# Kernel tuning notes

Hardware: AMD Instinct MI355X
Metric: run time of the kernel (lower is better)

The kernel has to match this reference:

```python
import jax, jax.numpy as jnp
import numpy as np

D_MODEL, D_STATE, EXPAND = 768, 16, 2
D_INNER = D_MODEL * EXPAND
B, L = 2, 2048


def setup_inputs() -> dict:
    key = jax.random.key(0)
    ks = jax.random.split(key, 10)
    s = 0.02  # init scale for projection weights
    return {
        "x": jax.random.normal(ks[0], (B, L, D_MODEL), jnp.float32),
        "in_w": jax.random.normal(ks[1], (D_MODEL, 2 * D_INNER), jnp.float32) * s,
        "conv_w": jax.random.normal(ks[2], (D_INNER, 1, 3), jnp.float32) * 0.1,
        "conv_b": jnp.zeros((D_INNER,), jnp.float32),
        "xproj_w": jax.random.normal(ks[3], (D_INNER, 2 * D_STATE), jnp.float32) * s,
        "dt_w": jax.random.normal(ks[4], (D_INNER, D_INNER), jnp.float32) * s,
        "dt_b": jnp.zeros((D_INNER,), jnp.float32),
        "A_log": jax.random.normal(ks[5], (D_INNER, D_STATE), jnp.float32) * 0.01,
        "D": jnp.ones((D_INNER,), jnp.float32),
        "out_w": jax.random.normal(ks[6], (D_INNER, D_MODEL), jnp.float32) * s,
    }


def reference(x, in_w, conv_w, conv_b, xproj_w, dt_w, dt_b, A_log, D, out_w):
    d_inner = conv_w.shape[0]
    d_state = A_log.shape[1]

    xz = x @ in_w                                   # [B,L,2*d_inner]
    x_c, z = jnp.split(xz, 2, axis=-1)

    # depthwise conv1d, kernel 3, padding 1
    xc = jnp.transpose(x_c, (0, 2, 1))              # [B,d_inner,L]
    xc = jax.lax.conv_general_dilated(
        xc, conv_w, window_strides=(1,), padding=[(1, 1)],
        feature_group_count=d_inner,
        dimension_numbers=("NCH", "OIH", "NCH"))
    xc = xc + conv_b[None, :, None]
    xc = jax.nn.silu(jnp.transpose(xc, (0, 2, 1)))  # [B,L,d_inner]

    Bs, Cs = jnp.split(xc @ xproj_w, 2, axis=-1)    # each [B,L,d_state]
    delta = jax.nn.softplus(xc @ dt_w + dt_b)       # [B,L,d_inner]
    A = -jnp.exp(A_log.astype(jnp.float32))         # [d_inner,d_state]

    deltaA = jnp.exp(jnp.einsum("bld,dn->bldn", delta, A))      # [B,L,d_inner,d_state]
    deltaBx = jnp.einsum("bld,bln->bldn", delta * xc, Bs)        # [B,L,d_inner,d_state]

    def step(h, inp):
        dA_t, dBx_t, c_t = inp                      # [B,d,n],[B,d,n],[B,n]
        h = dA_t * h + dBx_t
        y_t = jnp.einsum("bdn,bn->bd", h, c_t)
        return h, y_t

    h0 = jnp.zeros((x.shape[0], d_inner, d_state), xc.dtype)
    xs = (jnp.moveaxis(deltaA, 1, 0), jnp.moveaxis(deltaBx, 1, 0), jnp.moveaxis(Cs, 1, 0))
    _, ys = jax.lax.scan(step, h0, xs)              # ys: [L,B,d_inner]
    y = jnp.moveaxis(ys, 0, 1) + D * xc             # skip connection

    y = y * jax.nn.silu(z)
    return y @ out_w                                # [B,L,d_model]
```

## Files before the change

kernel.cpp:

```cpp
#include <hip/hip_runtime.h>
#include <cmath>

#define DMODEL 768
#define DINNER 1536
#define NSTATE 16
#define SEQL   2048
#define NCHUNK 32
#define CHLEN  64

#define DT_F32  0
#define DT_BF16 1
#define DT_ZERO 2

typedef __bf16 bf16x8 __attribute__((ext_vector_type(8)));
typedef float  f32x4  __attribute__((ext_vector_type(4)));

typedef __attribute__((address_space(3))) unsigned short lds_us;
typedef const __attribute__((address_space(1))) unsigned short glob_us;

__device__ __forceinline__ void async_cp16(glob_us* g, lds_us* l) {
    __builtin_amdgcn_global_load_lds((const __attribute__((address_space(1))) void*)g,
                                     (__attribute__((address_space(3))) void*)l, 16, 0, 0);
}

__device__ __forceinline__ float bf2f(unsigned short h) {
    union { unsigned u; float f; } v; v.u = ((unsigned)h) << 16; return v.f;
}
__device__ __forceinline__ float bflo(unsigned p) {
    union { unsigned u; float f; } v; v.u = p << 16; return v.f;
}
__device__ __forceinline__ float bfhi(unsigned p) {
    union { unsigned u; float f; } v; v.u = p & 0xFFFF0000u; return v.f;
}
__device__ __forceinline__ unsigned short f2bf(float f) {
    union { float f; unsigned u; } v; v.f = f;
    unsigned r = (v.u + 0x7FFFu + ((v.u >> 16) & 1u)) >> 16;
    return (unsigned short)r;
}
__device__ __forceinline__ float quad_reduce(float y) {
    int yi = __float_as_int(y);
    y += __int_as_float(__builtin_amdgcn_mov_dpp(yi, 0xB1, 0xF, 0xF, true));
    yi = __float_as_int(y);
    y += __int_as_float(__builtin_amdgcn_mov_dpp(yi, 0x4E, 0xF, 0xF, true));
    return y;
}
__device__ int detect_dtype(const void* p) {
    const unsigned* u = (const unsigned*)p;
    int nzlo = 0, band = 0, anynz = 0;
    for (int i = 0; i < 64; ++i) {
        unsigned w = u[i];
        anynz |= (w != 0);
        unsigned lo = w & 0xFFFFu;
        if (lo) {
            ++nzlo;
            unsigned e8 = (lo >> 7) & 0xFF;
            if (e8 >= 0x60 && e8 <= 0x8E) ++band;
        }
    }
    if (nzlo >= 8) return (band * 2 > nzlo) ? DT_BF16 : DT_F32;
    return anynz ? DT_F32 : DT_ZERO;
}
__device__ __forceinline__ float LD(const void* p, size_t i, int dt) {
    if (dt == DT_BF16) return bf2f(((const unsigned short*)p)[i]);
    if (dt == DT_F32)  return ((const float*)p)[i];
    return 0.f;
}

__global__ __launch_bounds__(256) void prep_kernel(
    const void* __restrict__ x, const void* __restrict__ in_w,
    const void* __restrict__ cw, const void* __restrict__ cb,
    const void* __restrict__ xp, const void* __restrict__ dt_w,
    const void* __restrict__ db, const void* __restrict__ Al,
    const void* __restrict__ Dv, const void* __restrict__ out_w,
    unsigned short* __restrict__ xb, unsigned short* __restrict__ inT,
    unsigned short* __restrict__ dtT, unsigned short* __restrict__ outT,
    unsigned short* __restrict__ xpT, float* __restrict__ pf)
{
    __shared__ unsigned short tile[64][68];
    __shared__ int dts[6];
    const int blk = blockIdx.x;
    const int t   = threadIdx.x;

    if (blk < 324) {
        if (t == 0) {
            dts[0] = detect_dtype(cw); dts[1] = detect_dtype(cb);
            dts[2] = detect_dtype(db); dts[3] = detect_dtype(Al);
            dts[4] = detect_dtype(Dv); dts[5] = detect_dtype(xp);
        }
        __syncthreads();
        int g = blk * 256 + t;
        if (g >= 82944) return;
        const void* src; int local; int which;
        if      (g <  4608) { src = cw; local = g;         which = 0; }
        else if (g <  6144) { src = cb; local = g - 4608;  which = 1; }
        else if (g <  7680) { src = db; local = g - 6144;  which = 2; }
        else if (g < 32256) { src = Al; local = g - 7680;  which = 3; }
        else if (g < 33792) { src = Dv; local = g - 32256; which = 4; }
        else                { src = xp; local = g - 33792; which = 5; }
        float v = LD(src, local, dts[which]);
        int out = g;
        if (which == 3) v = -__expf(v) * 1.44269504f;
        if (which == 0) out = (local % 3) * DINNER + local / 3;
        pf[out] = v;
    } else if (blk < 1860) {
        if (t == 0) dts[0] = detect_dtype(x);
        __syncthreads();
        const int dt = dts[0];
        size_t i = ((size_t)(blk - 324) * 256 + t) * 8;
        ushort4 o0, o1;
        if (dt == DT_F32) {
            float4 a = *(const float4*)((const float*)x + i);
            float4 b = *(const float4*)((const float*)x + i + 4);
            o0.x = f2bf(a.x); o0.y = f2bf(a.y); o0.z = f2bf(a.z); o0.w = f2bf(a.w);
            o1.x = f2bf(b.x); o1.y = f2bf(b.y); o1.z = f2bf(b.z); o1.w = f2bf(b.w);
        } else if (dt == DT_BF16) {
            o0 = *(const ushort4*)((const unsigned short*)x + i);
            o1 = *(const ushort4*)((const unsigned short*)x + i + 4);
        } else {
            o0 = (ushort4){0,0,0,0}; o1 = (ushort4){0,0,0,0};
        }
        *(ushort4*)&xb[i] = o0;
        *(ushort4*)&xb[i + 4] = o1;
    } else if (blk < 3300) {
        const void* src; unsigned short* dst; int R, C, tx_n, idx;
        if (blk < 2436)      { src = in_w;  dst = inT;  R = 768;  C = 3072; tx_n = 48; idx = blk - 1860; }
        else if (blk < 3012) { src = dt_w;  dst = dtT;  R = 1536; C = 1536; tx_n = 24; idx = blk - 2436; }
        else                 { src = out_w; dst = outT; R = 1536; C = 768;  tx_n = 12; idx = blk - 3012; }
        if (t == 0) dts[0] = detect_dtype(src);
        __syncthreads();
        const int dt = dts[0];
        const int tx = t & 15, ty = t >> 4;
        const int bx = (idx % tx_n) * 64, by = (idx / tx_n) * 64;
        #pragma unroll
        for (int i = 0; i < 4; ++i) {
            int rl = ty + i * 16;
            size_t soff = (size_t)(by + rl) * C + bx + tx * 4;
            ushort4 hv;
            if (dt == DT_F32) {
                float4 v = *(const float4*)((const float*)src + soff);
                hv.x = f2bf(v.x); hv.y = f2bf(v.y); hv.z = f2bf(v.z); hv.w = f2bf(v.w);
            } else if (dt == DT_BF16) {
                hv = *(const ushort4*)((const unsigned short*)src + soff);
            } else {
                hv = (ushort4){0,0,0,0};
            }
            *(ushort4*)&tile[rl][tx * 4] = hv;
        }
        __syncthreads();
        #pragma unroll
        for (int i = 0; i < 4; ++i) {
            int cl = ty + i * 16;
            int m0 = tx * 4;
            ushort4 o;
            o.x = tile[m0 + 0][cl]; o.y = tile[m0 + 1][cl];
            o.z = tile[m0 + 2][cl]; o.w = tile[m0 + 3][cl];
            *(ushort4*)&dst[(size_t)(bx + cl) * R + by + m0] = o;
        }
    } else {
        if (t == 0) dts[0] = detect_dtype(xp);
        __syncthreads();
        const int dt = dts[0];
        int r = (blk - 3300) * 256 + t;
        #pragma unroll 4
        for (int c = 0; c < 32; ++c) {
            float v = LD(xp, (size_t)r * 32 + c, dt);
            xpT[(size_t)c * DINNER + r] = f2bf(v);
        }
    }
}

template<int EPI>
__global__ __launch_bounds__(256) void gemm_kernel(
    const unsigned short* __restrict__ A, const unsigned short* __restrict__ Bt,
    void* __restrict__ C0, void* __restrict__ C1, const float* __restrict__ biasf,
    int M, int N, int K)
{
    __shared__ __align__(16) unsigned short As[2][2][128 * 32];
    __shared__ __align__(16) unsigned short Bs[2][2][64 * 32];
    const int t    = threadIdx.x;
    const int m0   = blockIdx.x * 128;
    const int n0   = blockIdx.y * 64;
    const int w    = t >> 6;
    const int lane = t & 63;
    const int wm   = (w >> 1) * 64, wn = (w & 1) * 32;
    const int lm   = lane & 15, quad = lane >> 4;
    const int srow = lane >> 2;
    const int sg   = lane & 3;

    f32x4 acc[4][2] = {};

    auto stage = [&](int k0, int q) {
        #pragma unroll
        for (int ph = 0; ph < 2; ++ph) {
            #pragma unroll
            for (int h = 0; h < 2; ++h) {
                int row = w * 32 + h * 16 + srow;
                int kg  = (sg - (row >> 1)) & 3;
                async_cp16((glob_us*)&A[(size_t)(m0 + row) * K + k0 + ph * 32 + kg * 8],
                           (lds_us*)&As[q][ph][(w * 32 + h * 16) * 32]);
            }
            int brow = w * 16 + srow;
            int bkg  = (sg - (brow >> 1)) & 3;
            async_cp16((glob_us*)&Bt[(size_t)(n0 + brow) * K + k0 + ph * 32 + bkg * 8],
                       (lds_us*)&Bs[q][ph][(w * 16) * 32]);
        }
    };

    stage(0, 0);

    int p = 0;
    for (int k0 = 0; k0 < K; k0 += 64) {
        __syncthreads();
        if (k0 + 64 < K) stage(k0 + 64, p ^ 1);
        #pragma unroll
        for (int ph = 0; ph < 2; ++ph) {
            bf16x8 af[4], bfr[2];
            #pragma unroll
            for (int i = 0; i < 4; ++i) {
                int row = wm + i * 16 + lm;
                int g   = (quad + (row >> 1)) & 3;
                af[i] = *(const bf16x8*)&As[p][ph][row * 32 + g * 8];
            }
            #pragma unroll
            for (int j = 0; j < 2; ++j) {
                int row = wn + j * 16 + lm;
                int g   = (quad + (row >> 1)) & 3;
                bfr[j] = *(const bf16x8*)&Bs[p][ph][row * 32 + g * 8];
            }
            #pragma unroll
            for (int i = 0; i < 4; ++i)
                #pragma unroll
                for (int j = 0; j < 2; ++j)
                    acc[i][j] = __builtin_amdgcn_mfma_f32_16x16x32_bf16(af[i], bfr[j], acc[i][j], 0, 0, 0);
        }
        p ^= 1;
    }

    const int half = N >> 1;
    #pragma unroll
    for (int i = 0; i < 4; ++i) {
        #pragma unroll
        for (int j = 0; j < 2; ++j) {
            int col = n0 + wn + j * 16 + lm;
            #pragma unroll
            for (int r = 0; r < 4; ++r) {
                int row = m0 + wm + i * 16 + quad * 4 + r;
                float v = acc[i][j][r];
                if (EPI == 2) {
                    ((float*)C0)[(size_t)row * N + col] = v;
                } else {
                    if (col < half) {
                        ((unsigned short*)C0)[(size_t)row * half + col] = f2bf(v);
                    } else {
                        float s = v / (1.f + __expf(-v));
                        ((unsigned short*)C1)[(size_t)row * half + col - half] = f2bf(s);
                    }
                }
            }
        }
    }
}

__global__ __launch_bounds__(256) void gemm_fused_kernel(
    const unsigned short* __restrict__ A, const unsigned short* __restrict__ Bt,
    const unsigned short* __restrict__ Bt2,
    unsigned short* __restrict__ C0, float* __restrict__ C1,
    const float* __restrict__ biasf, int M, int K)
{
    __shared__ __align__(16) unsigned short As[2][128 * 32];
    __shared__ __align__(16) unsigned short Bs[2][64 * 32];
    const int t    = threadIdx.x;
    const int m0   = blockIdx.x * 128;
    const int n0   = blockIdx.y * 64;
    const int w    = t >> 6;
    const int lane = t & 63;
    const int wm   = (w >> 1) * 64, wn = (w & 1) * 32;
    const int lm   = lane & 15, quad = lane >> 4;
    const int srow = lane >> 2;
    const int sg   = lane & 3;

    const int arow0 = w * 32 + srow;
    const int arow1 = w * 32 + 16 + srow;
    const int akg0  = (sg - (arow0 >> 1)) & 3;
    const int akg1  = (sg - (arow1 >> 1)) & 3;
    const int brow  = w * 16 + srow;
    const int bkg   = (sg - (brow >> 1)) & 3;
    const int gr    = n0 + brow;
    const unsigned short* aB0 = &A[(size_t)(m0 + arow0) * K + akg0 * 8];
    const unsigned short* aB1 = &A[(size_t)(m0 + arow1) * K + akg1 * 8];
    const unsigned short* bB  = (gr < 1536)
        ? &Bt[(size_t)gr * K + bkg * 8]
        : &Bt2[(size_t)(((gr < 1567) ? gr : 1567) - 1536) * K + bkg * 8];

    f32x4 acc[4][2] = {};

    auto stage = [&](int k0, int q) {
        async_cp16((glob_us*)(aB0 + k0), (lds_us*)&As[q][(w * 32) * 32]);
        async_cp16((glob_us*)(aB1 + k0), (lds_us*)&As[q][(w * 32 + 16) * 32]);
        async_cp16((glob_us*)(bB  + k0), (lds_us*)&Bs[q][(w * 16) * 32]);
    };

    stage(0, 0);

    int p = 0;
    for (int k0 = 0; k0 < K; k0 += 32) {
        __syncthreads();
        if (k0 + 32 < K) stage(k0 + 32, p ^ 1);
        bf16x8 af[4], bfr[2];
        #pragma unroll
        for (int i = 0; i < 4; ++i) {
            int row = wm + i * 16 + lm;
            int g   = (quad + (row >> 1)) & 3;
            af[i] = *(const bf16x8*)&As[p][row * 32 + g * 8];
        }
        #pragma unroll
        for (int j = 0; j < 2; ++j) {
            int row = wn + j * 16 + lm;
            int g   = (quad + (row >> 1)) & 3;
            bfr[j] = *(const bf16x8*)&Bs[p][row * 32 + g * 8];
        }
        #pragma unroll
        for (int i = 0; i < 4; ++i)
            #pragma unroll
            for (int j = 0; j < 2; ++j)
                acc[i][j] = __builtin_amdgcn_mfma_f32_16x16x32_bf16(af[i], bfr[j], acc[i][j], 0, 0, 0);
        p ^= 1;
    }

    #pragma unroll
    for (int i = 0; i < 4; ++i) {
        #pragma unroll
        for (int j = 0; j < 2; ++j) {
            int col = n0 + wn + j * 16 + lm;
            #pragma unroll
            for (int r = 0; r < 4; ++r) {
                int row = m0 + wm + i * 16 + quad * 4 + r;
                float v = acc[i][j][r];
                if (col < 1536) {
                    v += biasf[col];
                    float sp = (v > 20.f) ? v : log1pf(__expf(v));
                    C0[(size_t)row * 1536 + col] = f2bf(sp);
                } else if (col < 1568) {
                    C1[(size_t)row * 32 + (col - 1536)] = v;
                }
            }
        }
    }
}

__global__ __launch_bounds__(256) void conv_silu_kernel(
    const unsigned short* __restrict__ xcpre, const float* __restrict__ cwf,
    const float* __restrict__ cbf, unsigned short* __restrict__ xcb)
{
    const float* cw0 = cwf;
    const float* cw1 = cwf + DINNER;
    const float* cw2 = cwf + 2 * DINNER;
    size_t idx = ((size_t)blockIdx.x * 256 + threadIdx.x) * 8;
    int d8  = (int)(idx % DINNER);
    int row = (int)(idx / DINNER);
    int l   = row % SEQL;
    size_t base = (size_t)row * DINNER + d8;
    uint4 zero = {0, 0, 0, 0};
    uint4 xm = (l > 0)        ? *(const uint4*)&xcpre[base - DINNER] : zero;
    uint4 x0 = *(const uint4*)&xcpre[base];
    uint4 xp = (l < SEQL - 1) ? *(const uint4*)&xcpre[base + DINNER] : zero;
    float4 c0a = *(const float4*)&cw0[d8], c0b = *(const float4*)&cw0[d8 + 4];
    float4 c1a = *(const float4*)&cw1[d8], c1b = *(const float4*)&cw1[d8 + 4];
    float4 c2a = *(const float4*)&cw2[d8], c2b = *(const float4*)&cw2[d8 + 4];
    float4 cba = *(const float4*)&cbf[d8], cbb = *(const float4*)&cbf[d8 + 4];
    const unsigned* mw = (const unsigned*)&xm;
    const unsigned* zw = (const unsigned*)&x0;
    const unsigned* pw = (const unsigned*)&xp;
    float w0[8] = {c0a.x, c0a.y, c0a.z, c0a.w, c0b.x, c0b.y, c0b.z, c0b.w};
    float w1[8] = {c1a.x, c1a.y, c1a.z, c1a.w, c1b.x, c1b.y, c1b.z, c1b.w};
    float w2[8] = {c2a.x, c2a.y, c2a.z, c2a.w, c2b.x, c2b.y, c2b.z, c2b.w};
    float bb[8] = {cba.x, cba.y, cba.z, cba.w, cbb.x, cbb.y, cbb.z, cbb.w};
    unsigned short out[8];
    #pragma unroll
    for (int k = 0; k < 8; ++k) {
        unsigned wm_ = mw[k >> 1], wz = zw[k >> 1], wp = pw[k >> 1];
        float a = (k & 1) ? bfhi(wm_) : bflo(wm_);
        float c = (k & 1) ? bfhi(wz)  : bflo(wz);
        float e = (k & 1) ? bfhi(wp)  : bflo(wp);
        float acc = bb[k] + a * w0[k] + c * w1[k] + e * w2[k];
        float s = acc / (1.f + __expf(-acc));
        out[k] = f2bf(s);
    }
    *(uint4*)&xcb[base] = *(uint4*)out;
}

struct GrpA { unsigned dv2[4], xv2[4]; f32x4 Bv[4]; };
struct GrpC { unsigned dv2[4], xv2[4]; f32x4 Bv[4], Cv[4]; };

__device__ __forceinline__ void ldA(GrpA& gp, const unsigned short* pd,
    const unsigned short* px, const float* pbc, int l) {
    #pragma unroll
    for (int j = 0; j < 4; ++j) {
        size_t o = (size_t)(l + j) * DINNER;
        gp.dv2[j] = *(const unsigned*)&pd[o];
        gp.xv2[j] = *(const unsigned*)&px[o];
        gp.Bv[j]  = *(const f32x4*)&pbc[(size_t)(l + j) * 32];
    }
}
__device__ __forceinline__ void ldC(GrpC& gp, const unsigned short* pd,
    const unsigned short* px, const float* pbc, int l) {
    #pragma unroll
    for (int j = 0; j < 4; ++j) {
        size_t o = (size_t)(l + j) * DINNER;
        gp.dv2[j] = *(const unsigned*)&pd[o];
        gp.xv2[j] = *(const unsigned*)&px[o];
        gp.Bv[j]  = *(const f32x4*)&pbc[(size_t)(l + j) * 32];
        gp.Cv[j]  = *(const f32x4*)&pbc[(size_t)(l + j) * 32 + 16];
    }
}
__device__ __forceinline__ void stepA(const GrpA& gp, const f32x4 A2a,
    const f32x4 A2b, f32x4& h0, f32x4& h1, float& sdv0, float& sdv1) {
    #pragma unroll
    for (int j = 0; j < 4; ++j) {
        float dv0 = bflo(gp.dv2[j]), dv1 = bfhi(gp.dv2[j]);
        float xv0 = bflo(gp.xv2[j]), xv1 = bfhi(gp.xv2[j]);
        sdv0 += dv0; sdv1 += dv1;
        f32x4 Bv = gp.Bv[j];
        f32x4 e0, e1;
        e0[0] = __builtin_amdgcn_exp2f(dv0 * A2a[0]);
        e0[1] = __builtin_amdgcn_exp2f(dv0 * A2a[1]);
        e0[2] = __builtin_amdgcn_exp2f(dv0 * A2a[2]);
        e0[3] = __builtin_amdgcn_exp2f(dv0 * A2a[3]);
        e1[0] = __builtin_amdgcn_exp2f(dv1 * A2b[0]);
        e1[1] = __builtin_amdgcn_exp2f(dv1 * A2b[1]);
        e1[2] = __builtin_amdgcn_exp2f(dv1 * A2b[2]);
        e1[3] = __builtin_amdgcn_exp2f(dv1 * A2b[3]);
        h0 = e0 * h0 + (dv0 * xv0) * Bv;
        h1 = e1 * h1 + (dv1 * xv1) * Bv;
    }
}

__global__ __launch_bounds__(256) void scan_phase_a(
    const unsigned short* __restrict__ dlt, const unsigned short* __restrict__ xcb,
    const float* __restrict__ BC, const float* __restrict__ A_log_f,
    unsigned short* __restrict__ P, float* __restrict__ S)
{
    const int t   = threadIdx.x;
    const int q   = t & 3;
    const int dpl = t >> 2;
    const int bid = blockIdx.x;
    const int dg  = bid % 12;
    const int cc  = (bid / 12) % NCHUNK;
    const int b   = bid / (12 * NCHUNK);
    const int d   = (dg * 64 + dpl) * 2;
    f32x4 A2a = *(const f32x4*)&A_log_f[d * 16 + q * 4];
    f32x4 A2b = *(const f32x4*)&A_log_f[(d + 1) * 16 + q * 4];
    f32x4 h0 = (f32x4){0.f, 0.f, 0.f, 0.f};
    f32x4 h1 = (f32x4){0.f, 0.f, 0.f, 0.f};
    float sdv0 = 0.f, sdv1 = 0.f;
    const int row0 = b * SEQL + cc * CHLEN;
    const unsigned short* pd = dlt + (size_t)row0 * DINNER + d;
    const unsigned short* px = xcb + (size_t)row0 * DINNER + d;
    const float* pbc = BC + (size_t)row0 * 32 + q * 4;

    GrpA ga, gb;
    ldA(ga, pd, px, pbc, 0);
    for (int l0 = 0; l0 < CHLEN; l0 += 8) {
        ldA(gb, pd, px, pbc, l0 + 4);
        stepA(ga, A2a, A2b, h0, h1, sdv0, sdv1);
        if (l0 + 8 < CHLEN) ldA(ga, pd, px, pbc, l0 + 8);
        stepA(gb, A2a, A2b, h0, h1, sdv0, sdv1);
    }

    size_t idx = (((size_t)(b * NCHUNK + cc)) * DINNER + d) * 16 + q * 4;
    *(f32x4*)&S[idx] = h0;
    *(f32x4*)&S[idx + 16] = h1;
    ushort4 p0, p1;
    p0.x = f2bf(__builtin_amdgcn_exp2f(sdv0 * A2a[0]));
    p0.y = f2bf(__builtin_amdgcn_exp2f(sdv0 * A2a[1]));
    p0.z = f2bf(__builtin_amdgcn_exp2f(sdv0 * A2a[2]));
    p0.w = f2bf(__builtin_amdgcn_exp2f(sdv0 * A2a[3]));
    p1.x = f2bf(__builtin_amdgcn_exp2f(sdv1 * A2b[0]));
    p1.y = f2bf(__builtin_amdgcn_exp2f(sdv1 * A2b[1]));
    p1.z = f2bf(__builtin_amdgcn_exp2f(sdv1 * A2b[2]));
    p1.w = f2bf(__builtin_amdgcn_exp2f(sdv1 * A2b[3]));
    *(ushort4*)&P[idx] = p0;
    *(ushort4*)&P[idx + 16] = p1;
}

__global__ __launch_bounds__(256) void scan_combine(
    const unsigned short* __restrict__ P, float* __restrict__ S)
{
    int t = blockIdx.x * 256 + threadIdx.x;
    int b = t / (DINNER * NSTATE);
    int dn = t % (DINNER * NSTATE);
    const size_t stride = (size_t)(DINNER * NSTATE);
    size_t idx = (size_t)b * NCHUNK * stride + dn;
    float Pv = bf2f(P[idx]);
    float Sv = S[idx];
    float H = 0.f;
    for (int c = 0; c < NCHUNK; ++c) {
        float Pn = 0.f, Sn = 0.f;
        if (c + 1 < NCHUNK) {
            Pn = bf2f(P[idx + stride]);
            Sn = S[idx + stride];
        }
        S[idx] = H;
        H = Pv * H + Sv;
        Pv = Pn; Sv = Sn;
        idx += stride;
    }
}

__global__ __launch_bounds__(256) void scan_phase_c(
    const unsigned short* __restrict__ dlt, const unsigned short* __restrict__ xcb,
    const float* __restrict__ BC, const unsigned short* __restrict__ zg,
    const float* __restrict__ A_log_f, const float* __restrict__ D_f,
    const float* __restrict__ Hin, unsigned short* __restrict__ yg)
{
    const int t   = threadIdx.x;
    const int q   = t & 3;
    const int dpl = t >> 2;
    const int bid = blockIdx.x;
    const int dg  = bid % 12;
    const int cc  = (bid / 12) % NCHUNK;
    const int b   = bid / (12 * NCHUNK);
    const int d   = (dg * 64 + dpl) * 2;
    f32x4 A2a = *(const f32x4*)&A_log_f[d * 16 + q * 4];
    f32x4 A2b = *(const f32x4*)&A_log_f[(d + 1) * 16 + q * 4];
    size_t hidx = (((size_t)(b * NCHUNK + cc)) * DINNER + d) * 16 + q * 4;
    f32x4 h0 = *(const f32x4*)&Hin[hidx];
    f32x4 h1 = *(const f32x4*)&Hin[hidx + 16];
    const float Dd0 = D_f[d], Dd1 = D_f[d + 1];
    const int row0 = b * SEQL + cc * CHLEN;
    const unsigned short* pd = dlt + (size_t)row0 * DINNER + d;
    const unsigned short* px = xcb + (size_t)row0 * DINNER + d;
    const unsigned short* pz = zg  + (size_t)row0 * DINNER + d;
    unsigned short* py = yg + (size_t)row0 * DINNER + d;
    const float* pbc = BC + (size_t)row0 * 32 + q * 4;

    GrpC ga, gb;
    auto stepC = [&](const GrpC& gp, int l) {
        #pragma unroll
        for (int j = 0; j < 4; ++j) {
            float dv0 = bflo(gp.dv2[j]), dv1 = bfhi(gp.dv2[j]);
            float xv0 = bflo(gp.xv2[j]), xv1 = bfhi(gp.xv2[j]);
            f32x4 Bv = gp.Bv[j], Cv = gp.Cv[j];
            f32x4 e0, e1;
            e0[0] = __builtin_amdgcn_exp2f(dv0 * A2a[0]);
            e0[1] = __builtin_amdgcn_exp2f(dv0 * A2a[1]);
            e0[2] = __builtin_amdgcn_exp2f(dv0 * A2a[2]);
            e0[3] = __builtin_amdgcn_exp2f(dv0 * A2a[3]);
            e1[0] = __builtin_amdgcn_exp2f(dv1 * A2b[0]);
            e1[1] = __builtin_amdgcn_exp2f(dv1 * A2b[1]);
            e1[2] = __builtin_amdgcn_exp2f(dv1 * A2b[2]);
            e1[3] = __builtin_amdgcn_exp2f(dv1 * A2b[3]);
            h0 = e0 * h0 + (dv0 * xv0) * Bv;
            h1 = e1 * h1 + (dv1 * xv1) * Bv;
            f32x4 y0v = h0 * Cv;
            f32x4 y1v = h1 * Cv;
            float y0 = quad_reduce(y0v[0] + y0v[1] + y0v[2] + y0v[3]);
            float y1 = quad_reduce(y1v[0] + y1v[1] + y1v[2] + y1v[3]);
            if (j == q) {
                unsigned zp = *(const unsigned*)&pz[(size_t)(l + j) * DINNER];
                ushort2 o;
                o.x = f2bf((y0 + Dd0 * xv0) * bflo(zp));
                o.y = f2bf((y1 + Dd1 * xv1) * bfhi(zp));
                *(ushort2*)&py[(size_t)(l + j) * DINNER] = o;
            }
        }
    };

    ldC(ga, pd, px, pbc, 0);
    for (int l0 = 0; l0 < CHLEN; l0 += 8) {
        ldC(gb, pd, px, pbc, l0 + 4);
        stepC(ga, l0);
        if (l0 + 8 < CHLEN) ldC(ga, pd, px, pbc, l0 + 8);
        stepC(gb, l0 + 4);
    }
}

__global__ void guard_kernel(float* out, int code)
{
    if (threadIdx.x == 0 && blockIdx.x == 0 && code) out[0] = (float)code;
}

extern "C" void kernel_launch(void* const* d_in, const int* in_sizes, int n_in,
                              void* d_out, int out_size, void* d_ws, size_t ws_size,
                              hipStream_t stream) {
    static const int EXPECTED[10] = {3145728, 2359296, 4608, 1536, 49152,
                                     2359296, 1536, 24576, 1536, 1179648};
    bool ok = (n_in == 10);
    if (ok) for (int i = 0; i < 10; ++i) ok = ok && (in_sizes[i] == EXPECTED[i]);
    int code = 0;
    if (!ok) code = 2000;
    else if (ws_size < 67895296ULL) code = 3000;
    if (code) { guard_kernel<<<1, 64, 0, stream>>>((float*)d_out, code); return; }

    const void* x       = d_in[0];
    const void* in_w    = d_in[1];
    const void* conv_w  = d_in[2];
    const void* conv_b  = d_in[3];
    const void* xproj_w = d_in[4];
    const void* dt_w    = d_in[5];
    const void* dt_b    = d_in[6];
    const void* A_log   = d_in[7];
    const void* Dvec    = d_in[8];
    const void* out_w   = d_in[9];

    char* ws = (char*)d_ws;
    float* conv_w_f = (float*)(ws + 0);
    float* conv_b_f = (float*)(ws + 18432);
    float* dt_b_f   = (float*)(ws + 24576);
    float* A_log_f  = (float*)(ws + 30720);
    float* D_f      = (float*)(ws + 129024);
    unsigned short* xpT   = (unsigned short*)(ws + 331776);
    unsigned short* xb    = (unsigned short*)(ws + 524288);
    unsigned short* inT   = (unsigned short*)(ws + 6815744);
    unsigned short* yg    = (unsigned short*)(ws + 524288);
    unsigned short* dtT   = (unsigned short*)(ws + 13107200);
    unsigned short* outT  = (unsigned short*)(ws + 17825792);
    unsigned short* xcpre = (unsigned short*)(ws + 20185088);
    unsigned short* dlt   = xcpre;
    float*          BC    = (float*)(ws + 32768000);
    unsigned short* zg    = (unsigned short*)(ws + 33292288);
    unsigned short* xcb   = (unsigned short*)(ws + 45875200);
    float*          scanS = (float*)(ws + 58458112);
    unsigned short* scanP = (unsigned short*)(ws + 64749568);

    prep_kernel<<<3306, 256, 0, stream>>>(x, in_w, conv_w, conv_b, xproj_w, dt_w,
                                          dt_b, A_log, Dvec, out_w,
                                          xb, inT, dtT, outT, xpT, (float*)ws);

    gemm_kernel<3><<<dim3(32, 48), 256, 0, stream>>>(xb, inT, (void*)xcpre,
                                                     (void*)zg, nullptr, 4096, 3072, 768);
    conv_silu_kernel<<<(4096 * DINNER / 8) / 256, 256, 0, stream>>>(xcpre, conv_w_f, conv_b_f, xcb);
    gemm_fused_kernel<<<dim3(32, 25), 256, 0, stream>>>(xcb, dtT, xpT, dlt, BC,
                                                        dt_b_f, 4096, 1536);
    scan_phase_a<<<768, 256, 0, stream>>>(dlt, xcb, BC, A_log_f, scanP, scanS);
    scan_combine<<<192, 256, 0, stream>>>(scanP, scanS);
    scan_phase_c<<<768, 256, 0, stream>>>(dlt, xcb, BC, zg, A_log_f, D_f, scanS, yg);
    gemm_kernel<2><<<dim3(32, 12), 256, 0, stream>>>(yg, outT, d_out,
                                                     nullptr, nullptr, 4096, 768, 1536);
}
```

Before: 299.7 us.

## Fuse scan phases into one kernel with inter-block flag synchronization

```diff
diff --git a/kernel.cpp b/kernel.cpp
--- a/kernel.cpp
+++ b/kernel.cpp
@@ -74,13 +74,18 @@
     const void* __restrict__ Dv, const void* __restrict__ out_w,
     unsigned short* __restrict__ xb, unsigned short* __restrict__ inT,
     unsigned short* __restrict__ dtT, unsigned short* __restrict__ outT,
-    unsigned short* __restrict__ xpT, float* __restrict__ pf)
+    unsigned short* __restrict__ xpT, int* __restrict__ flags,
+    float* __restrict__ pf)
 {
     __shared__ unsigned short tile[64][68];
     __shared__ int dts[6];
     const int blk = blockIdx.x;
     const int t   = threadIdx.x;
 
+    if (blk == 3306) {
+        if (t < 768) flags[t] = 0;
+        return;
+    }
     if (blk < 324) {
         if (t == 0) {
             dts[0] = detect_dtype(cw); dts[1] = detect_dtype(cb);
@@ -435,10 +440,12 @@
     }
 }
 
-__global__ __launch_bounds__(256) void scan_phase_a(
+__global__ __launch_bounds__(256, 4) void scan_fused(
     const unsigned short* __restrict__ dlt, const unsigned short* __restrict__ xcb,
-    const float* __restrict__ BC, const float* __restrict__ A_log_f,
-    unsigned short* __restrict__ P, float* __restrict__ S)
+    const float* __restrict__ BC, const unsigned short* __restrict__ zg,
+    const float* __restrict__ A_log_f, const float* __restrict__ D_f,
+    unsigned short* __restrict__ P, float* __restrict__ S,
+    int* __restrict__ flags, unsigned short* __restrict__ yg)
 {
     const int t   = threadIdx.x;
     const int q   = t & 3;
@@ -450,89 +457,77 @@
     const int d   = (dg * 64 + dpl) * 2;
     f32x4 A2a = *(const f32x4*)&A_log_f[d * 16 + q * 4];
     f32x4 A2b = *(const f32x4*)&A_log_f[(d + 1) * 16 + q * 4];
-    f32x4 h0 = (f32x4){0.f, 0.f, 0.f, 0.f};
-    f32x4 h1 = (f32x4){0.f, 0.f, 0.f, 0.f};
-    float sdv0 = 0.f, sdv1 = 0.f;
     const int row0 = b * SEQL + cc * CHLEN;
     const unsigned short* pd = dlt + (size_t)row0 * DINNER + d;
     const unsigned short* px = xcb + (size_t)row0 * DINNER + d;
     const float* pbc = BC + (size_t)row0 * 32 + q * 4;
 
-    GrpA ga, gb;
-    ldA(ga, pd, px, pbc, 0);
-    for (int l0 = 0; l0 < CHLEN; l0 += 8) {
-        ldA(gb, pd, px, pbc, l0 + 4);
-        stepA(ga, A2a, A2b, h0, h1, sdv0, sdv1);
-        if (l0 + 8 < CHLEN) ldA(ga, pd, px, pbc, l0 + 8);
-        stepA(gb, A2a, A2b, h0, h1, sdv0, sdv1);
+    f32x4 h0 = (f32x4){0.f, 0.f, 0.f, 0.f};
+    f32x4 h1 = (f32x4){0.f, 0.f, 0.f, 0.f};
+    float sdv0 = 0.f, sdv1 = 0.f;
+    {
+        GrpA ga, gb;
+        ldA(ga, pd, px, pbc, 0);
+        for (int l0 = 0; l0 < CHLEN; l0 += 8) {
+            ldA(gb, pd, px, pbc, l0 + 4);
+            stepA(ga, A2a, A2b, h0, h1, sdv0, sdv1);
+            if (l0 + 8 < CHLEN) ldA(ga, pd, px, pbc, l0 + 8);
+            stepA(gb, A2a, A2b, h0, h1, sdv0, sdv1);
+        }
     }
 
     size_t idx = (((size_t)(b * NCHUNK + cc)) * DINNER + d) * 16 + q * 4;
     *(f32x4*)&S[idx] = h0;
     *(f32x4*)&S[idx + 16] = h1;
-    ushort4 p0, p1;
-    p0.x = f2bf(__builtin_amdgcn_exp2f(sdv0 * A2a[0]));
-    p0.y = f2bf(__builtin_amdgcn_exp2f(sdv0 * A2a[1]));
-    p0.z = f2bf(__builtin_amdgcn_exp2f(sdv0 * A2a[2]));
-    p0.w = f2bf(__builtin_amdgcn_exp2f(sdv0 * A2a[3]));
-    p1.x = f2bf(__builtin_amdgcn_exp2f(sdv1 * A2b[0]));
-    p1.y = f2bf(__builtin_amdgcn_exp2f(sdv1 * A2b[1]));
-    p1.z = f2bf(__builtin_amdgcn_exp2f(sdv1 * A2b[2]));
-    p1.w = f2bf(__builtin_amdgcn_exp2f(sdv1 * A2b[3]));
-    *(ushort4*)&P[idx] = p0;
-    *(ushort4*)&P[idx + 16] = p1;
-}
-
-__global__ __launch_bounds__(256) void scan_combine(
-    const unsigned short* __restrict__ P, float* __restrict__ S)
-{
-    int t = blockIdx.x * 256 + threadIdx.x;
-    int b = t / (DINNER * NSTATE);
-    int dn = t % (DINNER * NSTATE);
-    const size_t stride = (size_t)(DINNER * NSTATE);
-    size_t idx = (size_t)b * NCHUNK * stride + dn;
-    float Pv = bf2f(P[idx]);
-    float Sv = S[idx];
-    float H = 0.f;
-    for (int c = 0; c < NCHUNK; ++c) {
-        float Pn = 0.f, Sn = 0.f;
-        if (c + 1 < NCHUNK) {
-            Pn = bf2f(P[idx + stride]);
-            Sn = S[idx + stride];
-        }
-        S[idx] = H;
-        H = Pv * H + Sv;
-        Pv = Pn; Sv = Sn;
-        idx += stride;
-    }
-}
-
-__global__ __launch_bounds__(256) void scan_phase_c(
-    const unsigned short* __restrict__ dlt, const unsigned short* __restrict__ xcb,
-    const float* __restrict__ BC, const unsigned short* __restrict__ zg,
-    const float* __restrict__ A_log_f, const float* __restrict__ D_f,
-    const float* __restrict__ Hin, unsigned short* __restrict__ yg)
-{
-    const int t   = threadIdx.x;
-    const int q   = t & 3;
-    const int dpl = t >> 2;
-    const int bid = blockIdx.x;
-    const int dg  = bid % 12;
-    const int cc  = (bid / 12) % NCHUNK;
-    const int b   = bid / (12 * NCHUNK);
-    const int d   = (dg * 64 + dpl) * 2;
-    f32x4 A2a = *(const f32x4*)&A_log_f[d * 16 + q * 4];
-    f32x4 A2b = *(const f32x4*)&A_log_f[(d + 1) * 16 + q * 4];
-    size_t hidx = (((size_t)(b * NCHUNK + cc)) * DINNER + d) * 16 + q * 4;
-    f32x4 h0 = *(const f32x4*)&Hin[hidx];
-    f32x4 h1 = *(const f32x4*)&Hin[hidx + 16];
+    {
+        ushort4 p0, p1;
+        p0.x = f2bf(__builtin_amdgcn_exp2f(sdv0 * A2a[0]));
+        p0.y = f2bf(__builtin_amdgcn_exp2f(sdv0 * A2a[1]));
+        p0.z = f2bf(__builtin_amdgcn_exp2f(sdv0 * A2a[2]));
+        p0.w = f2bf(__builtin_amdgcn_exp2f(sdv0 * A2a[3]));
+        p1.x = f2bf(__builtin_amdgcn_exp2f(sdv1 * A2b[0]));
+        p1.y = f2bf(__builtin_amdgcn_exp2f(sdv1 * A2b[1]));
+        p1.z = f2bf(__builtin_amdgcn_exp2f(sdv1 * A2b[2]));
+        p1.w = f2bf(__builtin_amdgcn_exp2f(sdv1 * A2b[3]));
+        *(ushort4*)&P[idx] = p0;
+        *(ushort4*)&P[idx + 16] = p1;
+    }
+    __threadfence();
+    __syncthreads();
+    if (t == 0) atomicExch(&flags[(b * NCHUNK + cc) * 12 + dg], 1);
+
+    f32x4 H0 = (f32x4){0.f, 0.f, 0.f, 0.f};
+    f32x4 H1 = (f32x4){0.f, 0.f, 0.f, 0.f};
+    if (cc > 0) {
+        if (t < cc) {
+            while (atomicAdd(&flags[(b * NCHUNK + t) * 12 + dg], 0) == 0)
+                __builtin_amdgcn_s_sleep(2);
+        }
+        __syncthreads();
+        __threadfence();
+        f32x4 cp0 = (f32x4){1.f, 1.f, 1.f, 1.f};
+        f32x4 cp1 = (f32x4){1.f, 1.f, 1.f, 1.f};
+        for (int j = cc - 1; j >= 0; --j) {
+            size_t jidx = (((size_t)(b * NCHUNK + j)) * DINNER + d) * 16 + q * 4;
+            f32x4 Sj0 = *(const f32x4*)&S[jidx];
+            f32x4 Sj1 = *(const f32x4*)&S[jidx + 16];
+            ushort4 Pj0 = *(const ushort4*)&P[jidx];
+            ushort4 Pj1 = *(const ushort4*)&P[jidx + 16];
+            H0 = H0 + cp0 * Sj0;
+            H1 = H1 + cp1 * Sj1;
+            f32x4 pj0, pj1;
+            pj0[0] = bf2f(Pj0.x); pj0[1] = bf2f(Pj0.y); pj0[2] = bf2f(Pj0.z); pj0[3] = bf2f(Pj0.w);
+            pj1[0] = bf2f(Pj1.x); pj1[1] = bf2f(Pj1.y); pj1[2] = bf2f(Pj1.z); pj1[3] = bf2f(Pj1.w);
+            cp0 = cp0 * pj0;
+            cp1 = cp1 * pj1;
+        }
+    }
+
+    h0 = H0;
+    h1 = H1;
     const float Dd0 = D_f[d], Dd1 = D_f[d + 1];
-    const int row0 = b * SEQL + cc * CHLEN;
-    const unsigned short* pd = dlt + (size_t)row0 * DINNER + d;
-    const unsigned short* px = xcb + (size_t)row0 * DINNER + d;
-    const unsigned short* pz = zg  + (size_t)row0 * DINNER + d;
+    const unsigned short* pz = zg + (size_t)row0 * DINNER + d;
     unsigned short* py = yg + (size_t)row0 * DINNER + d;
-    const float* pbc = BC + (size_t)row0 * 32 + q * 4;
 
     GrpC ga, gb;
     auto stepC = [&](const GrpC& gp, int l) {
@@ -610,6 +605,7 @@
     float* A_log_f  = (float*)(ws + 30720);
     float* D_f      = (float*)(ws + 129024);
     unsigned short* xpT   = (unsigned short*)(ws + 331776);
+    int*            flags = (int*)(ws + 430080);
     unsigned short* xb    = (unsigned short*)(ws + 524288);
     unsigned short* inT   = (unsigned short*)(ws + 6815744);
     unsigned short* yg    = (unsigned short*)(ws + 524288);
@@ -623,18 +619,17 @@
     float*          scanS = (float*)(ws + 58458112);
     unsigned short* scanP = (unsigned short*)(ws + 64749568);
 
-    prep_kernel<<<3306, 256, 0, stream>>>(x, in_w, conv_w, conv_b, xproj_w, dt_w,
+    prep_kernel<<<3307, 256, 0, stream>>>(x, in_w, conv_w, conv_b, xproj_w, dt_w,
                                           dt_b, A_log, Dvec, out_w,
-                                          xb, inT, dtT, outT, xpT, (float*)ws);
+                                          xb, inT, dtT, outT, xpT, flags, (float*)ws);
 
     gemm_kernel<3><<<dim3(32, 48), 256, 0, stream>>>(xb, inT, (void*)xcpre,
                                                      (void*)zg, nullptr, 4096, 3072, 768);
     conv_silu_kernel<<<(4096 * DINNER / 8) / 256, 256, 0, stream>>>(xcpre, conv_w_f, conv_b_f, xcb);
     gemm_fused_kernel<<<dim3(32, 25), 256, 0, stream>>>(xcb, dtT, xpT, dlt, BC,
                                                         dt_b_f, 4096, 1536);
-    scan_phase_a<<<768, 256, 0, stream>>>(dlt, xcb, BC, A_log_f, scanP, scanS);
-    scan_combine<<<192, 256, 0, stream>>>(scanP, scanS);
-    scan_phase_c<<<768, 256, 0, stream>>>(dlt, xcb, BC, zg, A_log_f, D_f, scanS, yg);
+    scan_fused<<<768, 256, 0, stream>>>(dlt, xcb, BC, zg, A_log_f, D_f,
+                                        scanP, scanS, flags, yg);
     gemm_kernel<2><<<dim3(32, 12), 256, 0, stream>>>(yg, outT, d_out,
                                                      nullptr, nullptr, 4096, 768, 1536);
 }
```

Measured after the change: 472.2 us. +57.6%, slower.
